# Kernel tuning notes

Measured on AMD Instinct MI355X. Metric: run time of the kernel, lower is better.

## Reference

```python
import jax, jax.numpy as jnp
import numpy as np

B, N, H, E, C = 32, 128, 8, 64, 16
D = H * E  # d_model


def auto_head_configs(n_heads, patch_num):
    candidates = set()
    for d in range(1, patch_num + 1):
        for K in (3, 5, 7):
            eff = (K - 1) * d + 1
            if eff <= patch_num and K <= patch_num and (K % 2 == 1):
                candidates.add((K, d, eff))
    gk = patch_num if patch_num % 2 == 1 else patch_num - 1
    gk = max(1, gk)
    candidates.add((gk, 1, gk))
    candidates = sorted(candidates, key=lambda x: (x[2], -x[0], x[1]))
    if not candidates:
        return [(1, 1)] * n_heads
    configs = []
    for h in range(n_heads):
        idx = round(h * (len(candidates) - 1) / max(1, n_heads - 1))
        idx = min(idx, len(candidates) - 1)
        configs.append((candidates[idx][0], candidates[idx][1]))
    return configs


def build_na_mask(n_heads, patch_num):
    mask = np.zeros((n_heads, patch_num, patch_num), dtype=bool)
    for h, (K, d) in enumerate(auto_head_configs(n_heads, patch_num)):
        pos = np.arange(patch_num)[:, None]                      # [N,1]
        ideal = pos + (np.arange(K) - K // 2) * d                # [N,K]
        valid = (ideal >= 0) & (ideal < patch_num)
        rows = np.broadcast_to(pos, ideal.shape)
        mask[h, rows[valid], ideal[valid]] = True
    return mask


def setup_inputs() -> dict:
    key = jax.random.key(0)
    kq, kk, kv, k1, k2 = jax.random.split(key, 5)
    return {
        "queries": jax.random.normal(kq, (B, N, H, E), dtype=jnp.float32),
        "keys": jax.random.normal(kk, (B, C, N, H, E), dtype=jnp.float32),
        "values": jax.random.normal(kv, (B, C, N, H, E), dtype=jnp.float32),
        "w1": jax.random.normal(k1, (D, D // 4), dtype=jnp.float32) * 0.02,
        "b1": jnp.zeros((D // 4,), dtype=jnp.float32),
        "w2": jax.random.normal(k2, (D // 4, 1), dtype=jnp.float32) * 0.02,
        "b2": jnp.zeros((1,), dtype=jnp.float32),
        "na_mask": jnp.asarray(build_na_mask(H, N)),  # [H,N,N] bool
    }


def reference(queries, keys, values, w1, b1, w2, b2, na_mask):
    Bb, Nn, Hh, Ee = queries.shape
    Cc = keys.shape[1]
    scale = Ee ** (-0.5)
    # per-exo-variable gate from mean-pooled values
    v_pool = values.mean(axis=2).reshape(Bb, Cc, Hh * Ee)           # [B,C,D]
    hid = jax.nn.gelu(v_pool @ w1 + b1, approximate=False)
    gate = jax.nn.sigmoid(hid @ w2 + b2)                             # [B,C,1]
    q = queries.transpose(0, 2, 1, 3)                                # [B,H,N,E]
    k_cat = keys.transpose(0, 3, 1, 2, 4).reshape(Bb, Hh, Cc * Nn, Ee)
    v_g = values * gate[:, :, :, None, None]                         # [B,C,N,H,E]
    v_cat = v_g.transpose(0, 3, 1, 2, 4).reshape(Bb, Hh, Cc * Nn, Ee)
    # mask [H,N,N] -> [H,N,C*N] (same neighborhood replicated per exo var)
    tmask = jnp.broadcast_to(na_mask[:, :, None, :], (Hh, Nn, Cc, Nn)).reshape(Hh, Nn, Cc * Nn)
    attn = jnp.einsum('bhne,bhme->bhnm', q, k_cat) * scale
    attn = jnp.where(tmask, attn, -jnp.inf)
    attn = jax.nn.softmax(attn, axis=-1)
    out = jnp.einsum('bhnm,bhme->bhne', attn, v_cat)
    return out.transpose(0, 2, 1, 3)                                 # [B,N,H,E]
```

## Files before the change

kernel.cpp:

```cpp
#include <hip/hip_runtime.h>
#include <hip/hip_bf16.h>
#include <math.h>

#define BB 32
#define NN 128
#define HH 8
#define EE 64
#define CC 16
#define DD 512

#define NEG_BIG (-1.0e30f)

__device__ __forceinline__ float bf2f(unsigned short u) {
    union { unsigned int i; float f; } x; x.i = ((unsigned int)u) << 16; return x.f;
}
__device__ __forceinline__ float bflo(unsigned int u) {
    union { unsigned int i; float f; } x; x.i = u << 16; return x.f;
}
__device__ __forceinline__ float bfhi(unsigned int u) {
    union { unsigned int i; float f; } x; x.i = u & 0xffff0000u; return x.f;
}
__device__ __forceinline__ unsigned short f2bf(float f) {
    union { float f; unsigned int i; } x; x.f = f;
    unsigned int r = x.i + 0x7fffu + ((x.i >> 16) & 1u);
    return (unsigned short)(r >> 16);
}

template <bool F32>
__device__ __forceinline__ float ldx(const void* p, int i) {
    if constexpr (F32) return ((const float*)p)[i];
    else               return bf2f(((const unsigned short*)p)[i]);
}

__device__ __forceinline__ void wave_lds_sync() {
    asm volatile("s_waitcnt lgkmcnt(0)" ::: "memory");
    __builtin_amdgcn_wave_barrier();
}

#define DIL_PACK 0x3F3717250E130501ull

__global__ void detect_dtype(const unsigned short* __restrict__ q, int* __restrict__ flag) {
    const int lane = threadIdx.x;
    int outliers = 0;
    #pragma unroll
    for (int i = 0; i < 16; ++i) {
        unsigned short u = q[(i * 64 + lane) * 2];
        int e = (u >> 7) & 0xFF;
        int sane = (e >= 101 && e <= 140) || ((u & 0x7FFFu) == 0);
        outliers += !sane;
    }
    #pragma unroll
    for (int m = 32; m >= 1; m >>= 1) outliers += __shfl_xor(outliers, m, 64);
    if (lane == 0) *flag = (outliers > 256) ? 1 : 0;
}

template <bool F32>
__device__ __forceinline__ void gate_body(
    const void* __restrict__ values, const void* __restrict__ w1,
    const void* __restrict__ b1, const void* __restrict__ w2,
    const void* __restrict__ b2, float* __restrict__ gate_out,
    float (&vps)[4][DD], float (&vp)[DD], float (&hidp)[4][DD / 4], float (&hid)[DD / 4])
{
    const int bc  = blockIdx.x;
    const int t   = threadIdx.x;
    const int grp = t >> 8;
    const int tt  = t & 255;
    float a0 = 0.f, a1 = 0.f;
    if constexpr (F32) {
        const float2* vb = (const float2*)((const float*)values + (size_t)bc * NN * DD)
                           + (size_t)(grp * 32) * (DD / 2);
        #pragma unroll 8
        for (int n = 0; n < 32; ++n) { float2 u = vb[n * (DD / 2) + tt]; a0 += u.x; a1 += u.y; }
    } else {
        const unsigned int* vb = (const unsigned int*)((const unsigned short*)values + (size_t)bc * NN * DD)
                                 + (size_t)(grp * 32) * (DD / 2);
        #pragma unroll 8
        for (int n = 0; n < 32; ++n) { unsigned int u = vb[n * (DD / 2) + tt]; a0 += bflo(u); a1 += bfhi(u); }
    }
    vps[grp][2 * tt]     = a0;
    vps[grp][2 * tt + 1] = a1;
    __syncthreads();
    if (t < 256) {
        float s0 = vps[0][2 * t]     + vps[1][2 * t]     + vps[2][2 * t]     + vps[3][2 * t];
        float s1 = vps[0][2 * t + 1] + vps[1][2 * t + 1] + vps[2][2 * t + 1] + vps[3][2 * t + 1];
        vp[2 * t]     = s0 * (1.0f / NN);
        vp[2 * t + 1] = s1 * (1.0f / NN);
    }
    __syncthreads();
    if (t < 512) {
        const int o  = t & 127;
        const int ch = t >> 7;
        float a = 0.f;
        #pragma unroll 4
        for (int dd = ch * 128; dd < ch * 128 + 128; ++dd)
            a += vp[dd] * ldx<F32>(w1, dd * (DD / 4) + o);
        hidp[ch][o] = a;
    }
    __syncthreads();
    if (t < 128) {
        float a = ldx<F32>(b1, t) + hidp[0][t] + hidp[1][t] + hidp[2][t] + hidp[3][t];
        hid[t] = 0.5f * a * (1.0f + erff(a * 0.70710678118654752440f));
    }
    __syncthreads();
    if (t < 64) {
        float s = hid[t] * ldx<F32>(w2, t) + hid[t + 64] * ldx<F32>(w2, t + 64);
        #pragma unroll
        for (int m = 32; m >= 1; m >>= 1) s += __shfl_xor(s, m, 64);
        if (t == 0) {
            float z = s + ldx<F32>(b2, 0);
            gate_out[bc] = 1.0f / (1.0f + expf(-z));
        }
    }
}

__global__ __launch_bounds__(1024) void gate_kernel(
    const void* __restrict__ values, const void* __restrict__ w1,
    const void* __restrict__ b1, const void* __restrict__ w2,
    const void* __restrict__ b2, const int* __restrict__ flag,
    float* __restrict__ gate_out)
{
    __shared__ float vps[4][DD];
    __shared__ float vp[DD];
    __shared__ float hidp[4][DD / 4];
    __shared__ float hid[DD / 4];
    if (*flag) gate_body<true >(values, w1, b1, w2, b2, gate_out, vps, vp, hidp, hid);
    else       gate_body<false>(values, w1, b1, w2, b2, gate_out, vps, vp, hidp, hid);
}

template <bool F32, int K>
__device__ __forceinline__ void attn_body(
    const void* __restrict__ qptr, const void* __restrict__ kptr,
    const void* __restrict__ vptr, const float* __restrict__ gate,
    void* __restrict__ optr,
    int b, int h, int n, int dil, int wave, int lane,
    float (&lds_w)[4][CC * 5])
{
    constexpr int PRE = (K == 3) ? 3 : 4;
    const int g   = lane >> 2;
    const int sub = lane & 3;

    const size_t qoff  = (((size_t)b * NN + n) * HH + h) * EE;
    const size_t kvoff = ((size_t)b * CC * NN) * DD + (size_t)h * EE;

    const float gv = gate[b * CC + g];

    int  jj[K];
    bool va[K];
    #pragma unroll
    for (int k = 0; k < K; ++k) {
        int j = n + (k - (K >> 1)) * dil;
        va[k] = (j >= 0) && (j < NN);
        jj[k] = j;
    }

    float qreg[16];
    if constexpr (F32) {
        const float4* qp = (const float4*)((const float*)qptr + qoff + sub * 16);
        #pragma unroll
        for (int i = 0; i < 4; ++i) {
            float4 u = qp[i];
            qreg[4 * i + 0] = u.x * 0.125f; qreg[4 * i + 1] = u.y * 0.125f;
            qreg[4 * i + 2] = u.z * 0.125f; qreg[4 * i + 3] = u.w * 0.125f;
        }
    } else {
        const uint4* qp = (const uint4*)((const unsigned short*)qptr + qoff + sub * 16);
        #pragma unroll
        for (int i = 0; i < 2; ++i) {
            uint4 u = qp[i];
            qreg[8 * i + 0] = bflo(u.x) * 0.125f; qreg[8 * i + 1] = bfhi(u.x) * 0.125f;
            qreg[8 * i + 2] = bflo(u.y) * 0.125f; qreg[8 * i + 3] = bfhi(u.y) * 0.125f;
            qreg[8 * i + 4] = bflo(u.z) * 0.125f; qreg[8 * i + 5] = bfhi(u.z) * 0.125f;
            qreg[8 * i + 6] = bflo(u.w) * 0.125f; qreg[8 * i + 7] = bfhi(u.w) * 0.125f;
        }
    }

    const size_t rowbase = kvoff + (size_t)g * NN * DD + (size_t)sub * 16;
    float s[K];
    #pragma unroll
    for (int k = 0; k < K; ++k) {
        s[k] = NEG_BIG;
        if (va[k]) {
            size_t off = rowbase + (size_t)jj[k] * DD;
            float a0 = 0.f, a1 = 0.f, a2 = 0.f, a3 = 0.f;
            if constexpr (F32) {
                const float4* kp = (const float4*)((const float*)kptr + off);
                #pragma unroll
                for (int i = 0; i < 4; ++i) {
                    float4 kk = kp[i];
                    a0 += qreg[4 * i + 0] * kk.x; a1 += qreg[4 * i + 1] * kk.y;
                    a2 += qreg[4 * i + 2] * kk.z; a3 += qreg[4 * i + 3] * kk.w;
                }
            } else {
                const uint4* kp = (const uint4*)((const unsigned short*)kptr + off);
                #pragma unroll
                for (int i = 0; i < 2; ++i) {
                    uint4 kk = kp[i];
                    a0 += qreg[8 * i + 0] * bflo(kk.x); a1 += qreg[8 * i + 1] * bfhi(kk.x);
                    a2 += qreg[8 * i + 2] * bflo(kk.y); a3 += qreg[8 * i + 3] * bfhi(kk.y);
                    a0 += qreg[8 * i + 4] * bflo(kk.z); a1 += qreg[8 * i + 5] * bfhi(kk.z);
                    a2 += qreg[8 * i + 6] * bflo(kk.w); a3 += qreg[8 * i + 7] * bfhi(kk.w);
                }
            }
            float t = (a0 + a1) + (a2 + a3);
            t += __shfl_xor(t, 1, 64);
            t += __shfl_xor(t, 2, 64);
            s[k] = t;
        }
    }

    float vv[PRE][CC];
    #pragma unroll
    for (int k = 0; k < PRE; ++k) {
        if (va[k]) {
            const size_t base = kvoff + (size_t)jj[k] * DD + lane;
            if constexpr (F32) {
                const float* vb = (const float*)vptr + base;
                #pragma unroll
                for (int c = 0; c < CC; ++c) vv[k][c] = vb[(size_t)c * (NN * DD)];
            } else {
                const unsigned short* vb = (const unsigned short*)vptr + base;
                #pragma unroll
                for (int c = 0; c < CC; ++c) vv[k][c] = bf2f(vb[(size_t)c * (NN * DD)]);
            }
        }
    }

    float m = s[0];
    #pragma unroll
    for (int k = 1; k < K; ++k) m = fmaxf(m, s[k]);
    #pragma unroll
    for (int mm = 4; mm <= 32; mm <<= 1) m = fmaxf(m, __shfl_xor(m, mm, 64));
    float e[K];
    float ts = 0.f;
    #pragma unroll
    for (int k = 0; k < K; ++k) {
        if (va[k]) { e[k] = expf(s[k] - m); ts += e[k]; }
    }
    #pragma unroll
    for (int mm = 4; mm <= 32; mm <<= 1) ts += __shfl_xor(ts, mm, 64);
    float inv = 1.0f / ts;
    if (sub == 0) {
        #pragma unroll
        for (int k = 0; k < K; ++k)
            if (va[k]) lds_w[wave][k * CC + g] = e[k] * inv * gv;
    }

    float vl[CC];
    if constexpr (K == 5) {
        if (va[K - 1]) {
            const size_t base = kvoff + (size_t)jj[K - 1] * DD + lane;
            if constexpr (F32) {
                const float* vb = (const float*)vptr + base;
                #pragma unroll
                for (int c = 0; c < CC; ++c) vl[c] = vb[(size_t)c * (NN * DD)];
            } else {
                const unsigned short* vb = (const unsigned short*)vptr + base;
                #pragma unroll
                for (int c = 0; c < CC; ++c) vl[c] = bf2f(vb[(size_t)c * (NN * DD)]);
            }
        }
    }

    wave_lds_sync();

    float acc = 0.f;
    #pragma unroll
    for (int k = 0; k < PRE; ++k) {
        if (va[k]) {
            const float4* w4 = (const float4*)(lds_w[wave] + k * CC);
            float4 w0 = w4[0], w1 = w4[1], w2 = w4[2], w3 = w4[3];
            acc += w0.x * vv[k][0]  + w0.y * vv[k][1]  + w0.z * vv[k][2]  + w0.w * vv[k][3];
            acc += w1.x * vv[k][4]  + w1.y * vv[k][5]  + w1.z * vv[k][6]  + w1.w * vv[k][7];
            acc += w2.x * vv[k][8]  + w2.y * vv[k][9]  + w2.z * vv[k][10] + w2.w * vv[k][11];
            acc += w3.x * vv[k][12] + w3.y * vv[k][13] + w3.z * vv[k][14] + w3.w * vv[k][15];
        }
    }
    if constexpr (K == 5) {
        if (va[K - 1]) {
            const float4* w4 = (const float4*)(lds_w[wave] + (K - 1) * CC);
            float4 w0 = w4[0], w1 = w4[1], w2 = w4[2], w3 = w4[3];
            acc += w0.x * vl[0]  + w0.y * vl[1]  + w0.z * vl[2]  + w0.w * vl[3];
            acc += w1.x * vl[4]  + w1.y * vl[5]  + w1.z * vl[6]  + w1.w * vl[7];
            acc += w2.x * vl[8]  + w2.y * vl[9]  + w2.z * vl[10] + w2.w * vl[11];
            acc += w3.x * vl[12] + w3.y * vl[13] + w3.z * vl[14] + w3.w * vl[15];
        }
    }
    if constexpr (F32) ((float*)optr)[qoff + lane] = acc;
    else               ((unsigned short*)optr)[qoff + lane] = f2bf(acc);
}

__global__ __launch_bounds__(256) void attn_kernel(
    const void* __restrict__ qptr, const void* __restrict__ kptr,
    const void* __restrict__ vptr, const float* __restrict__ gate,
    const int* __restrict__ flag, void* __restrict__ optr)
{
    __shared__ float lds_w[4][CC * 5];
    const int tid  = threadIdx.x;
    const int wave = tid >> 6;
    const int lane = tid & 63;

    const int p    = blockIdx.x;
    const int virt = ((p & 7) << 10) | (p >> 3);
    const int gw0  = virt * 4;
    const int n    = (gw0 & (NN - 1)) + wave;
    const int h    = (gw0 >> 7) & (HH - 1);
    const int b    = gw0 >> 10;
    const int dil  = (int)((DIL_PACK >> (h * 8)) & 0xFF);
    const bool k5  = (h & 1) && (h != 7);

    const int f = *flag;
    if (f) {
        if (k5) attn_body<true, 5>(qptr, kptr, vptr, gate, optr, b, h, n, dil, wave, lane, lds_w);
        else    attn_body<true, 3>(qptr, kptr, vptr, gate, optr, b, h, n, dil, wave, lane, lds_w);
    } else {
        if (k5) attn_body<false, 5>(qptr, kptr, vptr, gate, optr, b, h, n, dil, wave, lane, lds_w);
        else    attn_body<false, 3>(qptr, kptr, vptr, gate, optr, b, h, n, dil, wave, lane, lds_w);
    }
}

extern "C" void kernel_launch(void* const* d_in, const int* in_sizes, int n_in,
                              void* d_out, int out_size, void* d_ws, size_t ws_size,
                              hipStream_t stream) {
    const void* queries = d_in[0];
    const void* keys    = d_in[1];
    const void* values  = d_in[2];
    const void* w1      = d_in[3];
    const void* b1      = d_in[4];
    const void* w2      = d_in[5];
    const void* b2      = d_in[6];

    int*   flag    = (int*)d_ws;
    float* gate_ws = (float*)d_ws + 64;

    hipLaunchKernelGGL(detect_dtype, dim3(1), dim3(64), 0, stream,
                       (const unsigned short*)queries, flag);
    hipLaunchKernelGGL(gate_kernel, dim3(BB * CC), dim3(1024), 0, stream,
                       values, w1, b1, w2, b2, flag, gate_ws);
    hipLaunchKernelGGL(attn_kernel, dim3(BB * HH * NN / 4), dim3(256), 0, stream,
                       queries, keys, values, gate_ws, flag, d_out);
}
```

Measured before the change: 338.6 us.

## Load V in same row-vector layout as K and reduce across groups by shuffles

The attention kernel now reads V with the same coalesced float4/uint4 layout used for K, where each lane holds 16 channels of one exo variable. It accumulates weighted V per lane and then combines the 16 exo variables with a butterfly of cross-lane shuffles that also transposes channels into an output position per lane. This removes the LDS weight exchange and the strided per-channel V gathers. Each wave now handles four query positions, so the grid shrinks by four, trading parallelism for more work per wave and more shuffle instructions.

Result: slower. 389.8 us (+15.1%).

```diff
diff --git a/kernel.cpp b/kernel.cpp
--- a/kernel.cpp
+++ b/kernel.cpp
@@ -30,11 +30,6 @@
 __device__ __forceinline__ float ldx(const void* p, int i) {
     if constexpr (F32) return ((const float*)p)[i];
     else               return bf2f(((const unsigned short*)p)[i]);
-}
-
-__device__ __forceinline__ void wave_lds_sync() {
-    asm volatile("s_waitcnt lgkmcnt(0)" ::: "memory");
-    __builtin_amdgcn_wave_barrier();
 }
 
 #define DIL_PACK 0x3F3717250E130501ull
@@ -128,21 +123,14 @@
 }
 
 template <bool F32, int K>
-__device__ __forceinline__ void attn_body(
+__device__ __forceinline__ void attn_one(
     const void* __restrict__ qptr, const void* __restrict__ kptr,
-    const void* __restrict__ vptr, const float* __restrict__ gate,
-    void* __restrict__ optr,
-    int b, int h, int n, int dil, int wave, int lane,
-    float (&lds_w)[4][CC * 5])
-{
-    constexpr int PRE = (K == 3) ? 3 : 4;
-    const int g   = lane >> 2;
-    const int sub = lane & 3;
-
-    const size_t qoff  = (((size_t)b * NN + n) * HH + h) * EE;
-    const size_t kvoff = ((size_t)b * CC * NN) * DD + (size_t)h * EE;
-
-    const float gv = gate[b * CC + g];
+    const void* __restrict__ vptr, float gv, void* __restrict__ optr,
+    int b, int h, int n, int dil, int lane, int g, int sub)
+{
+    const size_t qoff    = (((size_t)b * NN + n) * HH + h) * EE;
+    const size_t kvoff   = ((size_t)b * CC * NN) * DD + (size_t)h * EE;
+    const size_t rowbase = kvoff + (size_t)g * NN * DD + (size_t)sub * 16;
 
     int  jj[K];
     bool va[K];
@@ -174,7 +162,6 @@
         }
     }
 
-    const size_t rowbase = kvoff + (size_t)g * NN * DD + (size_t)sub * 16;
     float s[K];
     #pragma unroll
     for (int k = 0; k < K; ++k) {
@@ -208,23 +195,6 @@
         }
     }
 
-    float vv[PRE][CC];
-    #pragma unroll
-    for (int k = 0; k < PRE; ++k) {
-        if (va[k]) {
-            const size_t base = kvoff + (size_t)jj[k] * DD + lane;
-            if constexpr (F32) {
-                const float* vb = (const float*)vptr + base;
-                #pragma unroll
-                for (int c = 0; c < CC; ++c) vv[k][c] = vb[(size_t)c * (NN * DD)];
-            } else {
-                const unsigned short* vb = (const unsigned short*)vptr + base;
-                #pragma unroll
-                for (int c = 0; c < CC; ++c) vv[k][c] = bf2f(vb[(size_t)c * (NN * DD)]);
-            }
-        }
-    }
-
     float m = s[0];
     #pragma unroll
     for (int k = 1; k < K; ++k) m = fmaxf(m, s[k]);
@@ -234,59 +204,74 @@
     float ts = 0.f;
     #pragma unroll
     for (int k = 0; k < K; ++k) {
+        e[k] = 0.f;
         if (va[k]) { e[k] = expf(s[k] - m); ts += e[k]; }
     }
     #pragma unroll
     for (int mm = 4; mm <= 32; mm <<= 1) ts += __shfl_xor(ts, mm, 64);
-    float inv = 1.0f / ts;
-    if (sub == 0) {
+    const float inv = 1.0f / ts;
+
+    float acc[16];
+    #pragma unroll
+    for (int t = 0; t < 16; ++t) acc[t] = 0.f;
+    #pragma unroll
+    for (int k = 0; k < K; ++k) {
+        if (va[k]) {
+            const float wk = e[k] * inv * gv;
+            size_t off = rowbase + (size_t)jj[k] * DD;
+            if constexpr (F32) {
+                const float4* vp4 = (const float4*)((const float*)vptr + off);
+                #pragma unroll
+                for (int i = 0; i < 4; ++i) {
+                    float4 v = vp4[i];
+                    acc[4 * i + 0] += wk * v.x; acc[4 * i + 1] += wk * v.y;
+                    acc[4 * i + 2] += wk * v.z; acc[4 * i + 3] += wk * v.w;
+                }
+            } else {
+                const uint4* vp4 = (const uint4*)((const unsigned short*)vptr + off);
+                #pragma unroll
+                for (int i = 0; i < 2; ++i) {
+                    uint4 v = vp4[i];
+                    acc[8 * i + 0] += wk * bflo(v.x); acc[8 * i + 1] += wk * bfhi(v.x);
+                    acc[8 * i + 2] += wk * bflo(v.y); acc[8 * i + 3] += wk * bfhi(v.y);
+                    acc[8 * i + 4] += wk * bflo(v.z); acc[8 * i + 5] += wk * bfhi(v.z);
+                    acc[8 * i + 6] += wk * bflo(v.w); acc[8 * i + 7] += wk * bfhi(v.w);
+                }
+            }
+        }
+    }
+
+    int nch = 16;
+    #pragma unroll
+    for (int L = 0; L < 4; ++L) {
+        nch >>= 1;
+        const int hi = (lane >> (2 + L)) & 1;
         #pragma unroll
-        for (int k = 0; k < K; ++k)
-            if (va[k]) lds_w[wave][k * CC + g] = e[k] * inv * gv;
-    }
-
-    float vl[CC];
-    if constexpr (K == 5) {
-        if (va[K - 1]) {
-            const size_t base = kvoff + (size_t)jj[K - 1] * DD + lane;
-            if constexpr (F32) {
-                const float* vb = (const float*)vptr + base;
-                #pragma unroll
-                for (int c = 0; c < CC; ++c) vl[c] = vb[(size_t)c * (NN * DD)];
-            } else {
-                const unsigned short* vb = (const unsigned short*)vptr + base;
-                #pragma unroll
-                for (int c = 0; c < CC; ++c) vl[c] = bf2f(vb[(size_t)c * (NN * DD)]);
+        for (int t = 0; t < 8; ++t) {
+            if (t < nch) {
+                float send = hi ? acc[t] : acc[t + nch];
+                float recv = __shfl_xor(send, 4 << L, 64);
+                acc[t] = (hi ? acc[t + nch] : acc[t]) + recv;
             }
         }
     }
-
-    wave_lds_sync();
-
-    float acc = 0.f;
-    #pragma unroll
-    for (int k = 0; k < PRE; ++k) {
-        if (va[k]) {
-            const float4* w4 = (const float4*)(lds_w[wave] + k * CC);
-            float4 w0 = w4[0], w1 = w4[1], w2 = w4[2], w3 = w4[3];
-            acc += w0.x * vv[k][0]  + w0.y * vv[k][1]  + w0.z * vv[k][2]  + w0.w * vv[k][3];
-            acc += w1.x * vv[k][4]  + w1.y * vv[k][5]  + w1.z * vv[k][6]  + w1.w * vv[k][7];
-            acc += w2.x * vv[k][8]  + w2.y * vv[k][9]  + w2.z * vv[k][10] + w2.w * vv[k][11];
-            acc += w3.x * vv[k][12] + w3.y * vv[k][13] + w3.z * vv[k][14] + w3.w * vv[k][15];
-        }
-    }
-    if constexpr (K == 5) {
-        if (va[K - 1]) {
-            const float4* w4 = (const float4*)(lds_w[wave] + (K - 1) * CC);
-            float4 w0 = w4[0], w1 = w4[1], w2 = w4[2], w3 = w4[3];
-            acc += w0.x * vl[0]  + w0.y * vl[1]  + w0.z * vl[2]  + w0.w * vl[3];
-            acc += w1.x * vl[4]  + w1.y * vl[5]  + w1.z * vl[6]  + w1.w * vl[7];
-            acc += w2.x * vl[8]  + w2.y * vl[9]  + w2.z * vl[10] + w2.w * vl[11];
-            acc += w3.x * vl[12] + w3.y * vl[13] + w3.z * vl[14] + w3.w * vl[15];
-        }
-    }
-    if constexpr (F32) ((float*)optr)[qoff + lane] = acc;
-    else               ((unsigned short*)optr)[qoff + lane] = f2bf(acc);
+    const int ch = sub * 16 + (((g & 1) << 3) | ((g & 2) << 1) | ((g & 4) >> 1) | ((g & 8) >> 3));
+    if constexpr (F32) ((float*)optr)[qoff + ch] = acc[0];
+    else               ((unsigned short*)optr)[qoff + ch] = f2bf(acc[0]);
+}
+
+template <bool F32, int K>
+__device__ __forceinline__ void attn_quad(
+    const void* __restrict__ qptr, const void* __restrict__ kptr,
+    const void* __restrict__ vptr, const float* __restrict__ gate,
+    void* __restrict__ optr, int b, int h, int n0, int dil, int lane)
+{
+    const int g   = lane >> 2;
+    const int sub = lane & 3;
+    const float gv = gate[b * CC + g];
+    #pragma unroll
+    for (int i = 0; i < 4; ++i)
+        attn_one<F32, K>(qptr, kptr, vptr, gv, optr, b, h, n0 + i, dil, lane, g, sub);
 }
 
 __global__ __launch_bounds__(256) void attn_kernel(
@@ -294,15 +279,14 @@
     const void* __restrict__ vptr, const float* __restrict__ gate,
     const int* __restrict__ flag, void* __restrict__ optr)
 {
-    __shared__ float lds_w[4][CC * 5];
     const int tid  = threadIdx.x;
     const int wave = tid >> 6;
     const int lane = tid & 63;
 
     const int p    = blockIdx.x;
-    const int virt = ((p & 7) << 10) | (p >> 3);
-    const int gw0  = virt * 4;
-    const int n    = (gw0 & (NN - 1)) + wave;
+    const int virt = ((p & 7) << 8) | (p >> 3);
+    const int gw0  = virt * 16;
+    const int n0   = (gw0 & (NN - 1)) + wave * 4;
     const int h    = (gw0 >> 7) & (HH - 1);
     const int b    = gw0 >> 10;
     const int dil  = (int)((DIL_PACK >> (h * 8)) & 0xFF);
@@ -310,11 +294,11 @@
 
     const int f = *flag;
     if (f) {
-        if (k5) attn_body<true, 5>(qptr, kptr, vptr, gate, optr, b, h, n, dil, wave, lane, lds_w);
-        else    attn_body<true, 3>(qptr, kptr, vptr, gate, optr, b, h, n, dil, wave, lane, lds_w);
+        if (k5) attn_quad<true, 5>(qptr, kptr, vptr, gate, optr, b, h, n0, dil, lane);
+        else    attn_quad<true, 3>(qptr, kptr, vptr, gate, optr, b, h, n0, dil, lane);
     } else {
-        if (k5) attn_body<false, 5>(qptr, kptr, vptr, gate, optr, b, h, n, dil, wave, lane, lds_w);
-        else    attn_body<false, 3>(qptr, kptr, vptr, gate, optr, b, h, n, dil, wave, lane, lds_w);
+        if (k5) attn_quad<false, 5>(qptr, kptr, vptr, gate, optr, b, h, n0, dil, lane);
+        else    attn_quad<false, 3>(qptr, kptr, vptr, gate, optr, b, h, n0, dil, lane);
     }
 }
 
@@ -336,6 +320,6 @@
                        (const unsigned short*)queries, flag);
     hipLaunchKernelGGL(gate_kernel, dim3(BB * CC), dim3(1024), 0, stream,
                        values, w1, b1, w2, b2, flag, gate_ws);
-    hipLaunchKernelGGL(attn_kernel, dim3(BB * HH * NN / 4), dim3(256), 0, stream,
+    hipLaunchKernelGGL(attn_kernel, dim3(BB * HH * NN / 16), dim3(256), 0, stream,
                        queries, keys, values, gate_ws, flag, d_out);
 }
```

## Vectorize value loads per lane and replace LDS weight exchange with shuffles

Applied to the files above, without the earlier changes.

The value gather is restructured so each lane loads 4 contiguous channels (float4 or 4 bf16) for 4 exo variables, instead of one scalar per channel across 16 variables. The softmax·gate weights are broadcast with __shfl instead of being staged through LDS, and partial sums are reduced across the variable groups with xor shuffles. Only 16 lanes then write a vector output. This cuts the number of load instructions and removes the LDS round trip, at the cost of extra shuffles and a cross-lane reduction.

Result: no change. 336.8 us (-0.5%).

```diff
diff --git a/kernel.cpp b/kernel.cpp
--- a/kernel.cpp
+++ b/kernel.cpp
@@ -30,11 +30,6 @@
 __device__ __forceinline__ float ldx(const void* p, int i) {
     if constexpr (F32) return ((const float*)p)[i];
     else               return bf2f(((const unsigned short*)p)[i]);
-}
-
-__device__ __forceinline__ void wave_lds_sync() {
-    asm volatile("s_waitcnt lgkmcnt(0)" ::: "memory");
-    __builtin_amdgcn_wave_barrier();
 }
 
 #define DIL_PACK 0x3F3717250E130501ull
@@ -132,12 +127,13 @@
     const void* __restrict__ qptr, const void* __restrict__ kptr,
     const void* __restrict__ vptr, const float* __restrict__ gate,
     void* __restrict__ optr,
-    int b, int h, int n, int dil, int wave, int lane,
-    float (&lds_w)[4][CC * 5])
+    int b, int h, int n, int dil, int lane)
 {
     constexpr int PRE = (K == 3) ? 3 : 4;
-    const int g   = lane >> 2;
-    const int sub = lane & 3;
+    const int g    = lane >> 2;
+    const int sub  = lane & 3;
+    const int crow = lane >> 4;
+    const int ch0  = (lane & 15) * 4;
 
     const size_t qoff  = (((size_t)b * NN + n) * HH + h) * EE;
     const size_t kvoff = ((size_t)b * CC * NN) * DD + (size_t)h * EE;
@@ -208,19 +204,17 @@
         }
     }
 
-    float vv[PRE][CC];
+    float4 vv[PRE][4];
+    uint2  vb16[PRE][4];
     #pragma unroll
     for (int k = 0; k < PRE; ++k) {
         if (va[k]) {
-            const size_t base = kvoff + (size_t)jj[k] * DD + lane;
-            if constexpr (F32) {
-                const float* vb = (const float*)vptr + base;
-                #pragma unroll
-                for (int c = 0; c < CC; ++c) vv[k][c] = vb[(size_t)c * (NN * DD)];
-            } else {
-                const unsigned short* vb = (const unsigned short*)vptr + base;
-                #pragma unroll
-                for (int c = 0; c < CC; ++c) vv[k][c] = bf2f(vb[(size_t)c * (NN * DD)]);
+            #pragma unroll
+            for (int i = 0; i < 4; ++i) {
+                size_t off = kvoff + (size_t)(4 * i + crow) * (NN * DD)
+                           + (size_t)jj[k] * DD + ch0;
+                if constexpr (F32) vv[k][i]   = *(const float4*)((const float*)vptr + off);
+                else               vb16[k][i] = *(const uint2*)((const unsigned short*)vptr + off);
             }
         }
     }
@@ -234,59 +228,62 @@
     float ts = 0.f;
     #pragma unroll
     for (int k = 0; k < K; ++k) {
+        e[k] = 0.f;
         if (va[k]) { e[k] = expf(s[k] - m); ts += e[k]; }
     }
     #pragma unroll
     for (int mm = 4; mm <= 32; mm <<= 1) ts += __shfl_xor(ts, mm, 64);
-    float inv = 1.0f / ts;
-    if (sub == 0) {
-        #pragma unroll
-        for (int k = 0; k < K; ++k)
-            if (va[k]) lds_w[wave][k * CC + g] = e[k] * inv * gv;
-    }
-
-    float vl[CC];
+    const float inv = 1.0f / ts;
+
+    float4 vl[4];
+    uint2  vl16[4];
     if constexpr (K == 5) {
         if (va[K - 1]) {
-            const size_t base = kvoff + (size_t)jj[K - 1] * DD + lane;
-            if constexpr (F32) {
-                const float* vb = (const float*)vptr + base;
-                #pragma unroll
-                for (int c = 0; c < CC; ++c) vl[c] = vb[(size_t)c * (NN * DD)];
-            } else {
-                const unsigned short* vb = (const unsigned short*)vptr + base;
-                #pragma unroll
-                for (int c = 0; c < CC; ++c) vl[c] = bf2f(vb[(size_t)c * (NN * DD)]);
+            #pragma unroll
+            for (int i = 0; i < 4; ++i) {
+                size_t off = kvoff + (size_t)(4 * i + crow) * (NN * DD)
+                           + (size_t)jj[K - 1] * DD + ch0;
+                if constexpr (F32) vl[i]   = *(const float4*)((const float*)vptr + off);
+                else               vl16[i] = *(const uint2*)((const unsigned short*)vptr + off);
             }
         }
     }
 
-    wave_lds_sync();
-
-    float acc = 0.f;
-    #pragma unroll
-    for (int k = 0; k < PRE; ++k) {
+    float acc0 = 0.f, acc1 = 0.f, acc2 = 0.f, acc3 = 0.f;
+    #pragma unroll
+    for (int k = 0; k < K; ++k) {
         if (va[k]) {
-            const float4* w4 = (const float4*)(lds_w[wave] + k * CC);
-            float4 w0 = w4[0], w1 = w4[1], w2 = w4[2], w3 = w4[3];
-            acc += w0.x * vv[k][0]  + w0.y * vv[k][1]  + w0.z * vv[k][2]  + w0.w * vv[k][3];
-            acc += w1.x * vv[k][4]  + w1.y * vv[k][5]  + w1.z * vv[k][6]  + w1.w * vv[k][7];
-            acc += w2.x * vv[k][8]  + w2.y * vv[k][9]  + w2.z * vv[k][10] + w2.w * vv[k][11];
-            acc += w3.x * vv[k][12] + w3.y * vv[k][13] + w3.z * vv[k][14] + w3.w * vv[k][15];
-        }
-    }
-    if constexpr (K == 5) {
-        if (va[K - 1]) {
-            const float4* w4 = (const float4*)(lds_w[wave] + (K - 1) * CC);
-            float4 w0 = w4[0], w1 = w4[1], w2 = w4[2], w3 = w4[3];
-            acc += w0.x * vl[0]  + w0.y * vl[1]  + w0.z * vl[2]  + w0.w * vl[3];
-            acc += w1.x * vl[4]  + w1.y * vl[5]  + w1.z * vl[6]  + w1.w * vl[7];
-            acc += w2.x * vl[8]  + w2.y * vl[9]  + w2.z * vl[10] + w2.w * vl[11];
-            acc += w3.x * vl[12] + w3.y * vl[13] + w3.z * vl[14] + w3.w * vl[15];
-        }
-    }
-    if constexpr (F32) ((float*)optr)[qoff + lane] = acc;
-    else               ((unsigned short*)optr)[qoff + lane] = f2bf(acc);
+            const float wk_own = e[k] * inv * gv;
+            #pragma unroll
+            for (int i = 0; i < 4; ++i) {
+                const float w = __shfl(wk_own, 16 * i + 4 * crow, 64);
+                if constexpr (F32) {
+                    const float4 v = (k < PRE) ? vv[k][i] : vl[i];
+                    acc0 += w * v.x; acc1 += w * v.y; acc2 += w * v.z; acc3 += w * v.w;
+                } else {
+                    const uint2 v = (k < PRE) ? vb16[k][i] : vl16[i];
+                    acc0 += w * bflo(v.x); acc1 += w * bfhi(v.x);
+                    acc2 += w * bflo(v.y); acc3 += w * bfhi(v.y);
+                }
+            }
+        }
+    }
+
+    acc0 += __shfl_xor(acc0, 16, 64); acc0 += __shfl_xor(acc0, 32, 64);
+    acc1 += __shfl_xor(acc1, 16, 64); acc1 += __shfl_xor(acc1, 32, 64);
+    acc2 += __shfl_xor(acc2, 16, 64); acc2 += __shfl_xor(acc2, 32, 64);
+    acc3 += __shfl_xor(acc3, 16, 64); acc3 += __shfl_xor(acc3, 32, 64);
+    if (lane < 16) {
+        if constexpr (F32) {
+            float4 r; r.x = acc0; r.y = acc1; r.z = acc2; r.w = acc3;
+            ((float4*)((float*)optr + qoff))[lane] = r;
+        } else {
+            uint2 r;
+            r.x = ((unsigned int)f2bf(acc1) << 16) | (unsigned int)f2bf(acc0);
+            r.y = ((unsigned int)f2bf(acc3) << 16) | (unsigned int)f2bf(acc2);
+            ((uint2*)((unsigned short*)optr + qoff))[lane] = r;
+        }
+    }
 }
 
 __global__ __launch_bounds__(256) void attn_kernel(
@@ -294,7 +291,6 @@
     const void* __restrict__ vptr, const float* __restrict__ gate,
     const int* __restrict__ flag, void* __restrict__ optr)
 {
-    __shared__ float lds_w[4][CC * 5];
     const int tid  = threadIdx.x;
     const int wave = tid >> 6;
     const int lane = tid & 63;
@@ -310,11 +306,11 @@
 
     const int f = *flag;
     if (f) {
-        if (k5) attn_body<true, 5>(qptr, kptr, vptr, gate, optr, b, h, n, dil, wave, lane, lds_w);
-        else    attn_body<true, 3>(qptr, kptr, vptr, gate, optr, b, h, n, dil, wave, lane, lds_w);
+        if (k5) attn_body<true, 5>(qptr, kptr, vptr, gate, optr, b, h, n, dil, lane);
+        else    attn_body<true, 3>(qptr, kptr, vptr, gate, optr, b, h, n, dil, lane);
     } else {
-        if (k5) attn_body<false, 5>(qptr, kptr, vptr, gate, optr, b, h, n, dil, wave, lane, lds_w);
-        else    attn_body<false, 3>(qptr, kptr, vptr, gate, optr, b, h, n, dil, wave, lane, lds_w);
+        if (k5) attn_body<false, 5>(qptr, kptr, vptr, gate, optr, b, h, n, dil, lane);
+        else    attn_body<false, 3>(qptr, kptr, vptr, gate, optr, b, h, n, dil, lane);
     }
 }
 
```
